# Kernel optimization log

Measured on AMD Instinct MI355X. Metric: run time of the kernel, lower is better.

## Reference

```python
import jax, jax.numpy as jnp
import numpy as np

EPS_ATTN = 1e-6
EPS_LN = 1e-5

def _layernorm(x, g, b):
    mu = jnp.mean(x, axis=-1, keepdims=True)
    var = jnp.mean(jnp.square(x - mu), axis=-1, keepdims=True)
    return (x - mu) * jax.lax.rsqrt(var + EPS_LN) * g + b

def _phi(x):
    return jax.nn.elu(x) + 1.0

def setup_inputs() -> dict:
    key = jax.random.key(0)
    ks = jax.random.split(key, 7)
    N, L, C = 4, 16384, 256
    s = 1.0 / np.sqrt(C)
    return {
        "x": jax.random.normal(ks[0], (N, L, C), dtype=jnp.float32),
        "Wq": jax.random.normal(ks[1], (C, C), dtype=jnp.float32) * s,
        "Wk": jax.random.normal(ks[2], (C, C), dtype=jnp.float32) * s,
        "Wv": jax.random.normal(ks[3], (C, C), dtype=jnp.float32) * s,
        "Wm": jax.random.normal(ks[4], (C, C), dtype=jnp.float32) * s,
        "W1": jax.random.normal(ks[5], (2 * C, C), dtype=jnp.float32) * (1.0 / np.sqrt(2 * C)),
        "W2": jax.random.normal(ks[6], (C, C), dtype=jnp.float32) * s,
        "g1": jnp.ones((C,), jnp.float32),
        "b1": jnp.zeros((C,), jnp.float32),
        "g2": jnp.ones((C,), jnp.float32),
        "b2": jnp.zeros((C,), jnp.float32),
    }

def reference(x, Wq, Wk, Wv, Wm, W1, W2, g1, b1, g2, b2):
    N, L, C = x.shape
    H = 8
    D = C // H
    # qkv projections -> [n, l, h, d]
    q = (x @ Wq).reshape(N, L, H, D)
    k = (x @ Wk).reshape(N, L, H, D)
    v = (x @ Wv).reshape(N, L, H, D)
    # linear attention (elu feature map)
    Q = _phi(q)
    K = _phi(k)
    v_scaled = v / L
    KV = jnp.einsum('nshd,nshv->nhdv', K, v_scaled)          # [n,h,d,d]
    Z = 1.0 / (jnp.einsum('nlhd,nhd->nlh', Q, K.sum(axis=1)) + EPS_ATTN)
    msg = jnp.einsum('nlhd,nhdv,nlh->nlhv', Q, KV, Z) * L    # [n,l,h,d]
    # merge + norm1
    msg = msg.reshape(N, L, C) @ Wm
    msg = _layernorm(msg, g1, b1)
    # mlp(cat[x, msg]) + norm2
    h = jax.nn.relu(jnp.concatenate([x, msg], axis=-1) @ W1)
    msg = _layernorm(h @ W2, g2, b2)
    return x + msg
```

## Files before the change

### kernel.cpp

```cpp
#include <hip/hip_runtime.h>
#include <hip/hip_bf16.h>
#include <math.h>

#define NB 4
#define LB 16384
#define CB 256
#define HB 8
#define DB 32
#define NLB (NB * LB)
#define SPLITS 32
#define SPLIT_ROWS (LB / SPLITS)

typedef unsigned short ushort_t;
typedef __attribute__((ext_vector_type(8))) short bf16x8;
typedef __attribute__((ext_vector_type(4))) float f32x4;

__device__ __forceinline__ ushort_t f2b(float f) {
  union { __hip_bfloat16 h; ushort_t u; } cv;
  cv.h = __float2bfloat16(f);
  return cv.u;
}
__device__ __forceinline__ float b2f(ushort_t u) {
  union { __hip_bfloat16 h; ushort_t u; } cv;
  cv.u = u;
  return __bfloat162float(cv.h);
}

template <int AF32>
__device__ __forceinline__ void gemm_core2(const void* A, int strideA,
                                           const ushort_t* __restrict__ WT,
                                           int strideB, short* As, short* Bs,
                                           f32x4 acc[4][4], int nk) {
  const int t = threadIdx.x;
  const int lane = t & 63;
  const int w = t >> 6, wr = w >> 2, wc = w & 3;
  const int q = lane >> 4, lr = lane & 15;
  for (int ks = 0; ks < nk; ++ks) {
    const int k0 = ks * 64;
    __syncthreads();
    #pragma unroll
    for (int rep = 0; rep < 2; ++rep) {
      int si = t + 512 * rep;
      int r = si >> 3, s = si & 7;
      int dst = r * 64 + ((s ^ (r & 7)) << 3);
      if (AF32) {
        const float* src = (const float*)A + (size_t)r * strideA + k0 + 8 * s;
        float4 fa = *(const float4*)src;
        float4 fb = *(const float4*)(src + 4);
        ushort_t tmp[8] = {f2b(fa.x), f2b(fa.y), f2b(fa.z), f2b(fa.w),
                           f2b(fb.x), f2b(fb.y), f2b(fb.z), f2b(fb.w)};
        *(uint4*)&As[dst] = *(const uint4*)tmp;
      } else {
        const ushort_t* src =
            (const ushort_t*)A + (size_t)r * strideA + k0 + 8 * s;
        *(uint4*)&As[dst] = *(const uint4*)src;
      }
    }
    #pragma unroll
    for (int rep = 0; rep < 4; ++rep) {
      int si = t + 512 * rep;
      int r = si >> 3, s = si & 7;
      int dst = r * 64 + ((s ^ (r & 7)) << 3);
      const ushort_t* src = WT + (size_t)r * strideB + k0 + 8 * s;
      *(uint4*)&Bs[dst] = *(const uint4*)src;
    }
    __syncthreads();
    #pragma unroll
    for (int kk = 0; kk < 2; ++kk) {
      bf16x8 af[4], bfr[4];
      const int s = 4 * kk + q;
      #pragma unroll
      for (int m = 0; m < 4; ++m) {
        int r = wr * 64 + 16 * m + lr;
        af[m] = *(const bf16x8*)&As[r * 64 + ((s ^ (r & 7)) << 3)];
      }
      #pragma unroll
      for (int nn = 0; nn < 4; ++nn) {
        int c = wc * 64 + 16 * nn + lr;
        bfr[nn] = *(const bf16x8*)&Bs[c * 64 + ((s ^ (c & 7)) << 3)];
      }
      #pragma unroll
      for (int m = 0; m < 4; ++m)
        #pragma unroll
        for (int nn = 0; nn < 4; ++nn)
          acc[m][nn] = __builtin_amdgcn_mfma_f32_16x16x32_bf16(
              af[m], bfr[nn], acc[m][nn], 0, 0, 0);
    }
  }
}

__device__ __forceinline__ void zero_acc(f32x4 acc[4][4]) {
  #pragma unroll
  for (int m = 0; m < 4; ++m)
    #pragma unroll
    for (int n = 0; n < 4; ++n) acc[m][n] = 0.0f;
}

__device__ __forceinline__ void store_bf16(f32x4 acc[4][4], ushort_t* out,
                                           int row0, int do_phi) {
  const int t = threadIdx.x;
  const int lane = t & 63, w = t >> 6, wr = w >> 2, wc = w & 3;
  const int q = lane >> 4, lr = lane & 15;
  #pragma unroll
  for (int m = 0; m < 4; ++m)
    #pragma unroll
    for (int nn = 0; nn < 4; ++nn) {
      int col = wc * 64 + 16 * nn + lr;
      #pragma unroll
      for (int reg = 0; reg < 4; ++reg) {
        int row = row0 + wr * 64 + 16 * m + 4 * q + reg;
        float v = acc[m][nn][reg];
        if (do_phi) v = (v > 0.f) ? v + 1.f : __expf(v);
        out[(size_t)row * 256 + col] = f2b(v);
      }
    }
}

__global__ __launch_bounds__(512) void qkv3_kernel(
    const float* __restrict__ x, const ushort_t* __restrict__ WqT,
    const ushort_t* __restrict__ WkT, const ushort_t* __restrict__ WvT,
    ushort_t* __restrict__ Qb, ushort_t* __restrict__ Kb,
    ushort_t* __restrict__ Vb) {
  __shared__ short As[128 * 64];
  __shared__ short Bs[256 * 64];
  const int row0 = blockIdx.x * 128;
  const float* Ax = x + (size_t)row0 * 256;
  f32x4 acc[4][4];

  zero_acc(acc);
  gemm_core2<1>(Ax, 256, WqT, 256, As, Bs, acc, 4);
  store_bf16(acc, Qb, row0, 1);
  zero_acc(acc);
  gemm_core2<1>(Ax, 256, WkT, 256, As, Bs, acc, 4);
  store_bf16(acc, Kb, row0, 1);
  zero_acc(acc);
  gemm_core2<1>(Ax, 256, WvT, 256, As, Bs, acc, 4);
  store_bf16(acc, Vb, row0, 0);
}

template <int RESID>
__global__ __launch_bounds__(512) void gemmln2(
    const ushort_t* __restrict__ A, const ushort_t* __restrict__ WT,
    const float* __restrict__ g, const float* __restrict__ bvec,
    const float* __restrict__ resid, void* Out) {
  __shared__ short As[128 * 64];
  __shared__ short Bs[256 * 64];
  __shared__ float p1[128][4], p2[128][4], mus[128], rns[128];
  const int row0 = blockIdx.x * 128;
  f32x4 acc[4][4];
  zero_acc(acc);
  gemm_core2<0>(A + (size_t)row0 * 256, 256, WT, 256, As, Bs, acc, 4);
  const int t = threadIdx.x;
  const int lane = t & 63, w = t >> 6, wr = w >> 2, wc = w & 3;
  const int q = lane >> 4, lr = lane & 15;
  #pragma unroll
  for (int m = 0; m < 4; ++m)
    #pragma unroll
    for (int reg = 0; reg < 4; ++reg) {
      float s1 = 0.f, s2 = 0.f;
      #pragma unroll
      for (int nn = 0; nn < 4; ++nn) {
        float v = acc[m][nn][reg];
        s1 += v;
        s2 += v * v;
      }
      #pragma unroll
      for (int msk = 8; msk >= 1; msk >>= 1) {
        s1 += __shfl_xor(s1, msk);
        s2 += __shfl_xor(s2, msk);
      }
      if (lr == 0) {
        int rl = wr * 64 + 16 * m + 4 * q + reg;
        p1[rl][wc] = s1;
        p2[rl][wc] = s2;
      }
    }
  __syncthreads();
  if (t < 128) {
    float a = 0.f, b = 0.f;
    #pragma unroll
    for (int ww = 0; ww < 4; ++ww) {
      a += p1[t][ww];
      b += p2[t][ww];
    }
    float mu = a * (1.f / 256.f);
    float var = b * (1.f / 256.f) - mu * mu;
    mus[t] = mu;
    rns[t] = rsqrtf(var + 1e-5f);
  }
  __syncthreads();
  #pragma unroll
  for (int m = 0; m < 4; ++m)
    #pragma unroll
    for (int nn = 0; nn < 4; ++nn) {
      int col = wc * 64 + 16 * nn + lr;
      float gv = g[col], bv = bvec[col];
      #pragma unroll
      for (int reg = 0; reg < 4; ++reg) {
        int rl = wr * 64 + 16 * m + 4 * q + reg;
        int row = row0 + rl;
        float v = (acc[m][nn][reg] - mus[rl]) * rns[rl] * gv + bv;
        if (RESID) {
          v += resid[(size_t)row * 256 + col];
          ((float*)Out)[(size_t)row * 256 + col] = v;
        } else {
          ((ushort_t*)Out)[(size_t)row * 256 + col] = f2b(v);
        }
      }
    }
}

__global__ __launch_bounds__(512) void mlp1_v2(const float* __restrict__ x,
                                               const ushort_t* __restrict__ m1,
                                               const ushort_t* __restrict__ W1T,
                                               ushort_t* __restrict__ H) {
  __shared__ short As[128 * 64];
  __shared__ short Bs[256 * 64];
  const int row0 = blockIdx.x * 128;
  f32x4 acc[4][4];
  zero_acc(acc);
  gemm_core2<1>(x + (size_t)row0 * 256, 256, W1T, 512, As, Bs, acc, 4);
  gemm_core2<0>(m1 + (size_t)row0 * 256, 256, W1T + 256, 512, As, Bs, acc, 4);
  const int t = threadIdx.x;
  const int lane = t & 63, w = t >> 6, wr = w >> 2, wc = w & 3;
  const int q = lane >> 4, lr = lane & 15;
  #pragma unroll
  for (int m = 0; m < 4; ++m)
    #pragma unroll
    for (int nn = 0; nn < 4; ++nn) {
      int col = wc * 64 + 16 * nn + lr;
      #pragma unroll
      for (int reg = 0; reg < 4; ++reg) {
        int row = row0 + wr * 64 + 16 * m + 4 * q + reg;
        H[(size_t)row * 256 + col] = f2b(fmaxf(acc[m][nn][reg], 0.f));
      }
    }
}

__global__ __launch_bounds__(256) void wtrans_kernel(const float* __restrict__ W,
                                                     ushort_t* __restrict__ WT,
                                                     int K, int N) {
  __shared__ float tile[64][65];
  const int t = threadIdx.x;
  const int bx = blockIdx.x, by = blockIdx.y;
  for (int i = t; i < 4096; i += 256) {
    int r = i >> 6, c = i & 63;
    tile[r][c] = W[(size_t)(by * 64 + r) * N + bx * 64 + c];
  }
  __syncthreads();
  for (int i = t; i < 4096; i += 256) {
    int r = i >> 6, c = i & 63;
    WT[(size_t)(bx * 64 + r) * K + by * 64 + c] = f2b(tile[c][r]);
  }
}

__global__ __launch_bounds__(256) void kv_partial_kernel(
    const ushort_t* __restrict__ K, const ushort_t* __restrict__ V,
    float* __restrict__ Pp) {
  __shared__ float Ksh[64][32];
  __shared__ float Vsh[64][32];
  const int nh = blockIdx.x;
  const int n = nh >> 3, h = nh & 7;
  const int l0 = n * LB + blockIdx.y * SPLIT_ROWS;
  const int t = threadIdx.x;
  const int d = t >> 3, vg = t & 7;
  float acc[4] = {0.f, 0.f, 0.f, 0.f};
  float ksacc = 0.f;
  for (int tile = 0; tile < SPLIT_ROWS / 64; ++tile) {
    __syncthreads();
    {
      int rr = t >> 2, c8 = t & 3;
      size_t base = (size_t)(l0 + tile * 64 + rr) * 256 + h * 32 + 8 * c8;
      uint4 kr = *(const uint4*)&K[base];
      uint4 vr = *(const uint4*)&V[base];
      const ushort_t* kp = (const ushort_t*)&kr;
      const ushort_t* vp = (const ushort_t*)&vr;
      #pragma unroll
      for (int e = 0; e < 8; ++e) {
        Ksh[rr][8 * c8 + e] = b2f(kp[e]);
        Vsh[rr][8 * c8 + e] = b2f(vp[e]);
      }
    }
    __syncthreads();
    for (int r = 0; r < 64; ++r) {
      float kv = Ksh[r][d];
      if (vg == 0) ksacc += kv;
      #pragma unroll
      for (int qq = 0; qq < 4; ++qq)
        acc[qq] = fmaf(kv, Vsh[r][vg * 4 + qq], acc[qq]);
    }
  }
  float* rec = Pp + (size_t)(blockIdx.y * (NB * HB) + nh) * 1056;
  #pragma unroll
  for (int qq = 0; qq < 4; ++qq) rec[d * 32 + vg * 4 + qq] = acc[qq];
  if (vg == 0) rec[1024 + d] = ksacc;
}

__global__ __launch_bounds__(256) void kv_final_kernel(
    const float* __restrict__ Pp, float* __restrict__ KV,
    float* __restrict__ KS) {
  const int nh = blockIdx.x;
  const int t = threadIdx.x;
  for (int i = t; i < 1056; i += 256) {
    float s = 0.f;
    for (int sp = 0; sp < SPLITS; ++sp)
      s += Pp[(size_t)(sp * (NB * HB) + nh) * 1056 + i];
    if (i < 1024)
      KV[(size_t)nh * 1024 + i] = s;
    else
      KS[nh * 32 + (i - 1024)] = s;
  }
}

__global__ __launch_bounds__(256) void msg_kernel(ushort_t* __restrict__ QM,
                                                  const float* __restrict__ KV,
                                                  const float* __restrict__ KS) {
  __shared__ float Qs[32][256];
  __shared__ float kvs[8][32][32];
  __shared__ float ks[8][32];
  __shared__ float zs[32][8];
  const int t = threadIdx.x;
  const int row0 = blockIdx.x * 32;
  const int n = row0 >> 14;
  #pragma unroll
  for (int j = 0; j < 4; ++j) {
    int fi = t + 256 * j;
    int rr = fi >> 5, g8 = fi & 31;
    uint4 raw = *(const uint4*)&QM[(size_t)(row0 + rr) * 256 + 8 * g8];
    const ushort_t* pr = (const ushort_t*)&raw;
    #pragma unroll
    for (int e = 0; e < 8; ++e) Qs[rr][8 * g8 + e] = b2f(pr[e]);
  }
  const float* KVn = KV + (size_t)n * (HB * DB * DB);
  #pragma unroll
  for (int r = 0; r < 8; ++r) {
    int fi = t + 256 * r;
    ((float4*)kvs)[fi] = ((const float4*)KVn)[fi];
  }
  ((float*)ks)[t] = KS[n * 256 + t];
  __syncthreads();
  {
    int l = t >> 3, h = t & 7;
    float dsum = 0.f;
    #pragma unroll
    for (int dd = 0; dd < 32; ++dd)
      dsum = fmaf(Qs[l][h * 32 + dd], ks[h][dd], dsum);
    zs[l][h] = 1.0f / (dsum + 1e-6f);
  }
  __syncthreads();
  const int c = t, h = c >> 5, v = c & 31;
  for (int l = 0; l < 32; ++l) {
    float s = 0.f;
    #pragma unroll
    for (int dd = 0; dd < 32; ++dd)
      s = fmaf(Qs[l][h * 32 + dd], kvs[h][dd][v], s);
    QM[(size_t)(row0 + l) * 256 + c] = f2b(s * zs[l][h]);
  }
}

extern "C" void kernel_launch(void* const* d_in, const int* in_sizes, int n_in,
                              void* d_out, int out_size, void* d_ws,
                              size_t ws_size, hipStream_t stream) {
  const float* x = (const float*)d_in[0];
  const float* Wq = (const float*)d_in[1];
  const float* Wk = (const float*)d_in[2];
  const float* Wv = (const float*)d_in[3];
  const float* Wm = (const float*)d_in[4];
  const float* W1 = (const float*)d_in[5];
  const float* W2 = (const float*)d_in[6];
  const float* g1 = (const float*)d_in[7];
  const float* b1 = (const float*)d_in[8];
  const float* g2 = (const float*)d_in[9];
  const float* b2 = (const float*)d_in[10];
  float* out = (float*)d_out;

  const size_t PE = (size_t)NLB * CB;
  ushort_t* Qb = (ushort_t*)d_out;
  ushort_t* Kb = (ushort_t*)((char*)d_out + PE * 2);

  char* wsb = (char*)d_ws;
  ushort_t* Vb = (ushort_t*)wsb;
  float* Pp = (float*)(wsb + PE * 2);
  float* KVb = Pp + (size_t)SPLITS * NB * HB * 1056;
  float* KSb = KVb + (size_t)NB * HB * DB * DB;
  ushort_t* WqT = (ushort_t*)(KSb + NB * HB * DB);
  ushort_t* WkT = WqT + 256 * 256;
  ushort_t* WvT = WkT + 256 * 256;
  ushort_t* WmT = WvT + 256 * 256;
  ushort_t* W2T = WmT + 256 * 256;
  ushort_t* W1T = W2T + 256 * 256;

  wtrans_kernel<<<dim3(4, 4), 256, 0, stream>>>(Wq, WqT, 256, 256);
  wtrans_kernel<<<dim3(4, 4), 256, 0, stream>>>(Wk, WkT, 256, 256);
  wtrans_kernel<<<dim3(4, 4), 256, 0, stream>>>(Wv, WvT, 256, 256);
  wtrans_kernel<<<dim3(4, 4), 256, 0, stream>>>(Wm, WmT, 256, 256);
  wtrans_kernel<<<dim3(4, 4), 256, 0, stream>>>(W2, W2T, 256, 256);
  wtrans_kernel<<<dim3(4, 8), 256, 0, stream>>>(W1, W1T, 512, 256);

  qkv3_kernel<<<NLB / 128, 512, 0, stream>>>(x, WqT, WkT, WvT, Qb, Kb, Vb);
  kv_partial_kernel<<<dim3(NB * HB, SPLITS), 256, 0, stream>>>(Kb, Vb, Pp);
  kv_final_kernel<<<NB * HB, 256, 0, stream>>>(Pp, KVb, KSb);
  msg_kernel<<<NLB / 32, 256, 0, stream>>>(Qb, KVb, KSb);
  gemmln2<0><<<NLB / 128, 512, 0, stream>>>(Qb, WmT, g1, b1, nullptr, Kb);
  mlp1_v2<<<NLB / 128, 512, 0, stream>>>(x, Kb, W1T, Vb);
  gemmln2<1><<<NLB / 128, 512, 0, stream>>>(Vb, W2T, g2, b2, x, out);
}
```

Before: 384.4 us.

## Use direct global-to-LDS loads and pre-convert x to bf16 for QKV

```diff
diff --git a/kernel.cpp b/kernel.cpp
--- a/kernel.cpp
+++ b/kernel.cpp
@@ -26,8 +26,14 @@
   return __bfloat162float(cv.h);
 }
 
+__device__ __forceinline__ void gload16(const void* g, void* l) {
+  __builtin_amdgcn_global_load_lds(
+      (const __attribute__((address_space(1))) void*)g,
+      (__attribute__((address_space(3))) void*)l, 16, 0, 0);
+}
+
 template <int AF32>
-__device__ __forceinline__ void gemm_core2(const void* A, int strideA,
+__device__ __forceinline__ void gemm_core3(const void* A, int strideA,
                                            const ushort_t* __restrict__ WT,
                                            int strideB, short* As, short* Bs,
                                            f32x4 acc[4][4], int nk) {
@@ -38,31 +44,37 @@
   for (int ks = 0; ks < nk; ++ks) {
     const int k0 = ks * 64;
     __syncthreads();
-    #pragma unroll
-    for (int rep = 0; rep < 2; ++rep) {
-      int si = t + 512 * rep;
-      int r = si >> 3, s = si & 7;
-      int dst = r * 64 + ((s ^ (r & 7)) << 3);
-      if (AF32) {
+    if (AF32) {
+      #pragma unroll
+      for (int rep = 0; rep < 2; ++rep) {
+        int si = t + 512 * rep;
+        int r = si >> 3, s = si & 7;
+        int dst = r * 64 + ((s ^ (r & 7)) << 3);
         const float* src = (const float*)A + (size_t)r * strideA + k0 + 8 * s;
         float4 fa = *(const float4*)src;
         float4 fb = *(const float4*)(src + 4);
         ushort_t tmp[8] = {f2b(fa.x), f2b(fa.y), f2b(fa.z), f2b(fa.w),
                            f2b(fb.x), f2b(fb.y), f2b(fb.z), f2b(fb.w)};
         *(uint4*)&As[dst] = *(const uint4*)tmp;
-      } else {
+      }
+    } else {
+      #pragma unroll
+      for (int rep = 0; rep < 2; ++rep) {
+        int chunk = w * 2 + rep;
+        int si = chunk * 64 + lane;
+        int r = si >> 3, s = si & 7;
         const ushort_t* src =
-            (const ushort_t*)A + (size_t)r * strideA + k0 + 8 * s;
-        *(uint4*)&As[dst] = *(const uint4*)src;
+            (const ushort_t*)A + (size_t)r * strideA + k0 + 8 * (s ^ (r & 7));
+        gload16(src, As + chunk * 512);
       }
     }
     #pragma unroll
     for (int rep = 0; rep < 4; ++rep) {
-      int si = t + 512 * rep;
+      int chunk = w * 4 + rep;
+      int si = chunk * 64 + lane;
       int r = si >> 3, s = si & 7;
-      int dst = r * 64 + ((s ^ (r & 7)) << 3);
-      const ushort_t* src = WT + (size_t)r * strideB + k0 + 8 * s;
-      *(uint4*)&Bs[dst] = *(const uint4*)src;
+      const ushort_t* src = WT + (size_t)r * strideB + k0 + 8 * (s ^ (r & 7));
+      gload16(src, Bs + chunk * 512);
     }
     __syncthreads();
     #pragma unroll
@@ -116,26 +128,36 @@
     }
 }
 
+__global__ __launch_bounds__(256) void xconv_kernel(const float* __restrict__ x,
+                                                    ushort_t* __restrict__ xb) {
+  size_t i = ((size_t)blockIdx.x * 256 + threadIdx.x) * 8;
+  float4 a = *(const float4*)&x[i];
+  float4 b = *(const float4*)&x[i + 4];
+  ushort_t tmp[8] = {f2b(a.x), f2b(a.y), f2b(a.z), f2b(a.w),
+                     f2b(b.x), f2b(b.y), f2b(b.z), f2b(b.w)};
+  *(uint4*)&xb[i] = *(const uint4*)tmp;
+}
+
 __global__ __launch_bounds__(512) void qkv3_kernel(
-    const float* __restrict__ x, const ushort_t* __restrict__ WqT,
+    ushort_t* __restrict__ xb, const ushort_t* __restrict__ WqT,
     const ushort_t* __restrict__ WkT, const ushort_t* __restrict__ WvT,
-    ushort_t* __restrict__ Qb, ushort_t* __restrict__ Kb,
-    ushort_t* __restrict__ Vb) {
+    ushort_t* __restrict__ Qb, ushort_t* __restrict__ Kb) {
   __shared__ short As[128 * 64];
   __shared__ short Bs[256 * 64];
   const int row0 = blockIdx.x * 128;
-  const float* Ax = x + (size_t)row0 * 256;
+  const ushort_t* Ax = xb + (size_t)row0 * 256;
   f32x4 acc[4][4];
 
   zero_acc(acc);
-  gemm_core2<1>(Ax, 256, WqT, 256, As, Bs, acc, 4);
+  gemm_core3<0>(Ax, 256, WqT, 256, As, Bs, acc, 4);
   store_bf16(acc, Qb, row0, 1);
   zero_acc(acc);
-  gemm_core2<1>(Ax, 256, WkT, 256, As, Bs, acc, 4);
+  gemm_core3<0>(Ax, 256, WkT, 256, As, Bs, acc, 4);
   store_bf16(acc, Kb, row0, 1);
   zero_acc(acc);
-  gemm_core2<1>(Ax, 256, WvT, 256, As, Bs, acc, 4);
-  store_bf16(acc, Vb, row0, 0);
+  gemm_core3<0>(Ax, 256, WvT, 256, As, Bs, acc, 4);
+  __syncthreads();
+  store_bf16(acc, xb, row0, 0);
 }
 
 template <int RESID>
@@ -149,7 +171,7 @@
   const int row0 = blockIdx.x * 128;
   f32x4 acc[4][4];
   zero_acc(acc);
-  gemm_core2<0>(A + (size_t)row0 * 256, 256, WT, 256, As, Bs, acc, 4);
+  gemm_core3<0>(A + (size_t)row0 * 256, 256, WT, 256, As, Bs, acc, 4);
   const int t = threadIdx.x;
   const int lane = t & 63, w = t >> 6, wr = w >> 2, wc = w & 3;
   const int q = lane >> 4, lr = lane & 15;
@@ -219,8 +241,8 @@
   const int row0 = blockIdx.x * 128;
   f32x4 acc[4][4];
   zero_acc(acc);
-  gemm_core2<1>(x + (size_t)row0 * 256, 256, W1T, 512, As, Bs, acc, 4);
-  gemm_core2<0>(m1 + (size_t)row0 * 256, 256, W1T + 256, 512, As, Bs, acc, 4);
+  gemm_core3<1>(x + (size_t)row0 * 256, 256, W1T, 512, As, Bs, acc, 4);
+  gemm_core3<0>(m1 + (size_t)row0 * 256, 256, W1T + 256, 512, As, Bs, acc, 4);
   const int t = threadIdx.x;
   const int lane = t & 63, w = t >> 6, wr = w >> 2, wc = w & 3;
   const int q = lane >> 4, lr = lane & 15;
@@ -379,7 +401,7 @@
   ushort_t* Kb = (ushort_t*)((char*)d_out + PE * 2);
 
   char* wsb = (char*)d_ws;
-  ushort_t* Vb = (ushort_t*)wsb;
+  ushort_t* Vxb = (ushort_t*)wsb;
   float* Pp = (float*)(wsb + PE * 2);
   float* KVb = Pp + (size_t)SPLITS * NB * HB * 1056;
   float* KSb = KVb + (size_t)NB * HB * DB * DB;
@@ -397,11 +419,12 @@
   wtrans_kernel<<<dim3(4, 4), 256, 0, stream>>>(W2, W2T, 256, 256);
   wtrans_kernel<<<dim3(4, 8), 256, 0, stream>>>(W1, W1T, 512, 256);
 
-  qkv3_kernel<<<NLB / 128, 512, 0, stream>>>(x, WqT, WkT, WvT, Qb, Kb, Vb);
-  kv_partial_kernel<<<dim3(NB * HB, SPLITS), 256, 0, stream>>>(Kb, Vb, Pp);
+  xconv_kernel<<<PE / 2048, 256, 0, stream>>>(x, Vxb);
+  qkv3_kernel<<<NLB / 128, 512, 0, stream>>>(Vxb, WqT, WkT, WvT, Qb, Kb);
+  kv_partial_kernel<<<dim3(NB * HB, SPLITS), 256, 0, stream>>>(Kb, Vxb, Pp);
   kv_final_kernel<<<NB * HB, 256, 0, stream>>>(Pp, KVb, KSb);
   msg_kernel<<<NLB / 32, 256, 0, stream>>>(Qb, KVb, KSb);
   gemmln2<0><<<NLB / 128, 512, 0, stream>>>(Qb, WmT, g1, b1, nullptr, Kb);
-  mlp1_v2<<<NLB / 128, 512, 0, stream>>>(x, Kb, W1T, Vb);
-  gemmln2<1><<<NLB / 128, 512, 0, stream>>>(Vb, W2T, g2, b2, x, out);
-}
+  mlp1_v2<<<NLB / 128, 512, 0, stream>>>(x, Kb, W1T, Vxb);
+  gemmln2<1><<<NLB / 128, 512, 0, stream>>>(Vxb, W2T, g2, b2, x, out);
+}
```

After: 395.2 us. 1.03x slower.
